# Optimization experiments

Measured on AMD Instinct MI355X. Metric: run time of the kernel, lower is better.

The kernel has to match this reference:

```python
import jax, jax.numpy as jnp
import numpy as np

STDS = np.array([0.1, 0.1, 0.2, 0.2], np.float32)
MEANS = np.array([0.0, 0.0, 0.0, 0.0], np.float32)
NMS_THRESH = 0.3  # cfg.TEST.NMS


def _decode_clip(boxes, deltas, iminfo):
    # boxes [R,4] (x1,y1,x2,y2), deltas [R,C,4] (unnormalized), iminfo [3]=(h,w,scale)
    w = boxes[:, 2] - boxes[:, 0] + 1.0
    h = boxes[:, 3] - boxes[:, 1] + 1.0
    cx = boxes[:, 0] + 0.5 * w
    cy = boxes[:, 1] + 0.5 * h
    pcx = deltas[..., 0] * w[:, None] + cx[:, None]
    pcy = deltas[..., 1] * h[:, None] + cy[:, None]
    pw = jnp.exp(deltas[..., 2]) * w[:, None]
    ph = jnp.exp(deltas[..., 3]) * h[:, None]
    x1 = pcx - 0.5 * pw
    y1 = pcy - 0.5 * ph
    x2 = pcx + 0.5 * pw
    y2 = pcy + 0.5 * ph
    x1 = jnp.clip(x1, 0.0, iminfo[1] - 1.0)
    x2 = jnp.clip(x2, 0.0, iminfo[1] - 1.0)
    y1 = jnp.clip(y1, 0.0, iminfo[0] - 1.0)
    y2 = jnp.clip(y2, 0.0, iminfo[0] - 1.0)
    return jnp.stack([x1, y1, x2, y2], axis=-1)  # [R,C,4]


def _nms_keep(boxes, valid):
    # boxes [R,4] sorted by score desc; valid [R] bool. Greedy hard NMS, fixed shape.
    b = jax.lax.stop_gradient(boxes)
    R = b.shape[0]
    x1, y1, x2, y2 = b[:, 0], b[:, 1], b[:, 2], b[:, 3]
    area = jnp.maximum(x2 - x1, 0.0) * jnp.maximum(y2 - y1, 0.0)
    xx1 = jnp.maximum(x1[:, None], x1[None, :])
    yy1 = jnp.maximum(y1[:, None], y1[None, :])
    xx2 = jnp.minimum(x2[:, None], x2[None, :])
    yy2 = jnp.minimum(y2[:, None], y2[None, :])
    inter = jnp.maximum(xx2 - xx1, 0.0) * jnp.maximum(yy2 - yy1, 0.0)
    iou = inter / (area[:, None] + area[None, :] - inter + 1e-9)
    ar = jnp.arange(R)
    def body(i, keep):
        sup = (iou[i] > NMS_THRESH) & (ar > i) & keep[i]
        return keep & ~sup
    return jax.lax.fori_loop(0, R, body, valid)


def _per_class(scores, boxes, thresh, cls_id):
    # scores [R], boxes [R,4], scalar thresh, scalar class id
    valid = scores > thresh
    s = jnp.where(valid, scores, -jnp.inf)
    order = jnp.argsort(-s)
    b = boxes[order]
    v = valid[order]
    keep = _nms_keep(b, v)
    dets = jnp.concatenate([b, jnp.full((b.shape[0], 1), cls_id, b.dtype)], axis=1)  # [R,5]
    return dets, keep


def _per_image(scores, pred_boxes, thr, num_pad):
    # scores [R,C], pred_boxes [R,C,4], thr [C]
    C = scores.shape[1]
    cls_ids = jnp.arange(1, C, dtype=scores.dtype)
    dets, keep = jax.vmap(_per_class, in_axes=(1, 1, 0, 0))(
        scores[:, 1:], pred_boxes[:, 1:], thr[1:], cls_ids)  # [C-1,R,5], [C-1,R]
    dets = dets.reshape(-1, 5)   # class-major order == torch.cat over classes
    keep = keep.reshape(-1)
    pos = jnp.cumsum(keep) - 1
    write = keep & (pos < num_pad)  # truncate to num_pad like the original
    idx = jnp.where(write, pos, num_pad)  # overflow bucket
    out = jnp.zeros((num_pad + 1, 5), dets.dtype).at[idx].add(
        dets * write[:, None].astype(dets.dtype))
    n = jnp.minimum(keep.sum(), num_pad)
    return out[:num_pad], n  # zero-padded [num_pad,5], count


def reference(cls_prob, rois, bbox_pred, im_info, per_class_threshold, num_classes):
    B, R, C = cls_prob.shape
    deltas = bbox_pred.reshape(B, R, C, 4) * STDS + MEANS
    pred = jax.vmap(_decode_clip)(rois[:, :, 1:5], deltas, im_info)  # [B,R,C,4]
    gt, n = jax.vmap(lambda s, p: _per_image(s, p, per_class_threshold, num_classes))(
        cls_prob, pred)
    return gt, n


def setup_inputs() -> dict:
    key = jax.random.key(0)
    B, R, C = 2, 1000, 81
    ks = jax.random.split(key, 6)
    cls_prob = jax.nn.softmax(2.0 * jax.random.normal(ks[0], (B, R, C)), axis=-1)
    cx = jax.random.uniform(ks[1], (B, R)) * 1200.0 + 50.0
    cy = jax.random.uniform(ks[2], (B, R)) * 700.0 + 50.0
    bw = jax.random.uniform(ks[3], (B, R)) * 300.0 + 16.0
    bh = jax.random.uniform(ks[4], (B, R)) * 300.0 + 16.0
    x1 = jnp.clip(cx - 0.5 * bw, 0.0, 1332.0)
    x2 = jnp.clip(cx + 0.5 * bw, 0.0, 1332.0)
    y1 = jnp.clip(cy - 0.5 * bh, 0.0, 799.0)
    y2 = jnp.clip(cy + 0.5 * bh, 0.0, 799.0)
    rois = jnp.concatenate([jnp.zeros((B, R, 1)), jnp.stack([x1, y1, x2, y2], -1)], -1)
    bbox_pred = 0.5 * jax.random.normal(ks[5], (B, R, 4 * C))
    im_info = jnp.tile(jnp.array([[800.0, 1333.0, 1.0]], jnp.float32), (B, 1))
    per_class_threshold = jnp.full((C,), 0.05, jnp.float32)
    return {"cls_prob": cls_prob, "rois": rois, "bbox_pred": bbox_pred,
            "im_info": im_info, "per_class_threshold": per_class_threshold,
            "num_classes": C}
```

## Files before the change

### kernel.cpp

```cpp
#include <hip/hip_runtime.h>
#include <math.h>

#define MAXC 256
#define NMS_T 0.3f

__global__ __launch_bounds__(256) void nms_fused_kernel(
    const float* __restrict__ cls_prob, const float* __restrict__ rois,
    const float* __restrict__ bbox_pred, const float* __restrict__ im_info,
    const float* __restrict__ thr, float* __restrict__ ws_boxes,
    int* __restrict__ ws_counts, float* __restrict__ gt,
    float* __restrict__ nout, int B, int R, int C)
{
    const int task = blockIdx.x;
    const int NC = C - 1;
    const int b = task / NC;
    const int c = 1 + (task % NC);
    const int tid = threadIdx.x;
    const int lane = tid & 63;
    const unsigned long long lane_lt = (1ull << lane) - 1ull;

    __shared__ float2 s_pair[MAXC];
    __shared__ float4 s_bx[MAXC];
    __shared__ float  s_area[MAXC];
    __shared__ unsigned long long s_keepw[4];
    __shared__ int s_cnt;
    __shared__ int s_flag;
    __shared__ int s_pcnt[128];
    __shared__ int s_poff[128];
    __shared__ int s_total;

    if (tid == 0) s_cnt = 0;
    __syncthreads();

    const float tc = thr[c];
    for (int r = tid; r < R; r += 256) {
        float s = cls_prob[((size_t)b * R + r) * C + c];
        if (s > tc) {
            int p = atomicAdd(&s_cnt, 1);
            if (p < MAXC) s_pair[p] = make_float2(s, __int_as_float(r));
        }
    }
    __syncthreads();
    int K = s_cnt; if (K > MAXC) K = MAXC;

    const float maxx = im_info[b * 3 + 1] - 1.0f;
    const float maxy = im_info[b * 3 + 0] - 1.0f;

    if (tid < K) {
        const float2 me = s_pair[tid];
        const float si = me.x;
        const int   ri = __float_as_int(me.y);
        int rank = 0;
        for (int j = 0; j < K; j++) {
            float2 pj = s_pair[j];
            rank += (pj.x > si) || (pj.x == si && __float_as_int(pj.y) < ri);
        }
        const float* rp = rois + ((size_t)b * R + ri) * 5;
        float rx1 = rp[1], ry1 = rp[2], rx2 = rp[3], ry2 = rp[4];
        float w  = rx2 - rx1 + 1.0f;
        float h  = ry2 - ry1 + 1.0f;
        float cx = rx1 + 0.5f * w;
        float cy = ry1 + 0.5f * h;
        const float4 dv = *(const float4*)(bbox_pred + (((size_t)b * R + ri) * C + c) * 4);
        float d0 = dv.x * 0.1f, d1 = dv.y * 0.1f;
        float d2 = dv.z * 0.2f, d3 = dv.w * 0.2f;
        float pcx = d0 * w + cx;
        float pcy = d1 * h + cy;
        float pw  = expf(d2) * w;
        float ph  = expf(d3) * h;
        float x1 = fminf(fmaxf(pcx - 0.5f * pw, 0.0f), maxx);
        float x2 = fminf(fmaxf(pcx + 0.5f * pw, 0.0f), maxx);
        float y1 = fminf(fmaxf(pcy - 0.5f * ph, 0.0f), maxy);
        float y2 = fminf(fmaxf(pcy + 0.5f * ph, 0.0f), maxy);
        s_bx[rank] = make_float4(x1, y1, x2, y2);
        s_area[rank] = fmaxf(x2 - x1, 0.0f) * fmaxf(y2 - y1, 0.0f);
    }
    __syncthreads();

    float* dst = ws_boxes + (size_t)task * C * 5;
    const float cid = (float)c;

    if (K <= 64) {
        if (tid < 64) {
            float4 bj = (lane < K) ? s_bx[lane] : make_float4(0.f, 0.f, 0.f, 0.f);
            float  aj = (lane < K) ? s_area[lane] : 0.0f;
            unsigned long long row = 0ull;
            for (int j = 0; j < K; j++) {
                float4 bb = s_bx[j];
                float  ab = s_area[j];
                float xx1 = fmaxf(bj.x, bb.x);
                float yy1 = fmaxf(bj.y, bb.y);
                float xx2 = fminf(bj.z, bb.z);
                float yy2 = fminf(bj.w, bb.w);
                float inter = fmaxf(xx2 - xx1, 0.0f) * fmaxf(yy2 - yy1, 0.0f);
                float iou = inter / (aj + ab - inter + 1e-9f);
                if (j > lane && iou > NMS_T) row |= (1ull << j);
            }
            unsigned int rlo32 = (unsigned int)(row & 0xffffffffull);
            unsigned int rhi32 = (unsigned int)(row >> 32);
            unsigned long long rem = (K >= 64) ? ~0ull
                                   : ((K > 0) ? ((1ull << K) - 1ull) : 0ull);
            unsigned long long keep = 0ull;
            while (rem) {
                int i = __builtin_ctzll(rem);
                keep |= (1ull << i);
                unsigned int lo = (unsigned int)__shfl((int)rlo32, i);
                unsigned int hi = (unsigned int)__shfl((int)rhi32, i);
                rem &= ~(((unsigned long long)hi << 32) | lo);
                rem &= ~(1ull << i);
            }
            if ((keep >> lane) & 1ull) {
                int pos = __popcll(keep & lane_lt);
                if (pos < C) {
                    dst[pos * 5 + 0] = bj.x;
                    dst[pos * 5 + 1] = bj.y;
                    dst[pos * 5 + 2] = bj.z;
                    dst[pos * 5 + 3] = bj.w;
                    dst[pos * 5 + 4] = cid;
                }
            }
            if (lane == 0) ws_counts[task] = __popcll(keep);
        }
    } else {
        int q = tid >> 6;
        int idx = q * 64 + lane;
        float4 bq = (idx < K) ? s_bx[idx] : make_float4(0.f, 0.f, 0.f, 0.f);
        float  aq = (idx < K) ? s_area[idx] : 0.0f;
        if (tid < 4) {
            int remk = K - tid * 64;
            s_keepw[tid] = (remk >= 64) ? ~0ull
                         : ((remk > 0) ? ((1ull << remk) - 1ull) : 0ull);
        }
        __syncthreads();
        for (int i = 0; i < K; i++) {
            if ((s_keepw[i >> 6] >> (i & 63)) & 1ull) {
                float4 bi = s_bx[i];
                float  ai = s_area[i];
                float xx1 = fmaxf(bi.x, bq.x);
                float yy1 = fmaxf(bi.y, bq.y);
                float xx2 = fminf(bi.z, bq.z);
                float yy2 = fminf(bi.w, bq.w);
                float inter = fmaxf(xx2 - xx1, 0.0f) * fmaxf(yy2 - yy1, 0.0f);
                float iou = inter / (ai + aq - inter + 1e-9f);
                bool sup = (idx < K) && (idx > i) && (iou > NMS_T);
                unsigned long long supm = __ballot(sup);
                if (supm && lane == 0) s_keepw[q] &= ~supm;
            }
            __syncthreads();
        }
        unsigned long long km = s_keepw[q];
        int base = 0;
        for (int w = 0; w < q; w++) base += __popcll(s_keepw[w]);
        if (idx < K && ((km >> lane) & 1ull)) {
            int pos = base + __popcll(km & lane_lt);
            if (pos < C) {
                dst[pos * 5 + 0] = bq.x;
                dst[pos * 5 + 1] = bq.y;
                dst[pos * 5 + 2] = bq.z;
                dst[pos * 5 + 3] = bq.w;
                dst[pos * 5 + 4] = cid;
            }
        }
        if (tid == 0) {
            int total = 0;
#pragma unroll
            for (int w = 0; w < 4; w++) total += __popcll(s_keepw[w]);
            ws_counts[task] = total;
        }
    }

    __syncthreads();
    __threadfence();
    if (tid == 0) {
        unsigned int old = atomicAdd((unsigned int*)&nout[b], 1u);
        s_flag = (old == (unsigned int)(NC - 1)) ||
                 (old == 0xAAAAAAAAu + (unsigned int)(NC - 1));
    }
    __syncthreads();
    if (!s_flag) return;
    __threadfence();

    const int P = C;
    if (tid < NC) s_pcnt[tid] = ws_counts[b * NC + tid];
    __syncthreads();
    if (tid < NC) {
        int acc = 0;
        for (int cc = 0; cc < NC; cc++) {
            int v = s_pcnt[cc];
            if (cc < tid) acc += v;
        }
        s_poff[tid] = acc;
        if (tid == NC - 1) s_total = acc + s_pcnt[tid];
    }
    __syncthreads();
    const int n = (s_total < P) ? s_total : P;

    for (int i = n * 5 + tid; i < P * 5; i += 256)
        gt[(size_t)b * P * 5 + i] = 0.0f;

    if (tid < n) {
        int pos = tid;
        int lo = 0, hi = NC - 1;
        while (lo < hi) {
            int mid = (lo + hi + 1) >> 1;
            if (s_poff[mid] <= pos) lo = mid; else hi = mid - 1;
        }
        int cc = lo;
        int k = pos - s_poff[cc];
        const float* src = ws_boxes + (((size_t)(b * NC + cc)) * P + k) * 5;
        float4 v = *(const float4*)src;
        float  v4 = src[4];
        float* d = gt + ((size_t)b * P + pos) * 5;
        d[0] = v.x; d[1] = v.y; d[2] = v.z; d[3] = v.w; d[4] = v4;
    }
    if (tid == 0) nout[b] = (float)n;
}

extern "C" void kernel_launch(void* const* d_in, const int* in_sizes, int n_in,
                              void* d_out, int out_size, void* d_ws, size_t ws_size,
                              hipStream_t stream) {
    const float* cls_prob  = (const float*)d_in[0];
    const float* rois      = (const float*)d_in[1];
    const float* bbox_pred = (const float*)d_in[2];
    const float* im_info   = (const float*)d_in[3];
    const float* thr       = (const float*)d_in[4];

    const int B = in_sizes[3] / 3;
    const int C = in_sizes[4];
    const int R = in_sizes[0] / (B * C);
    const int NC = C - 1;

    float* ws_boxes = (float*)d_ws;
    int*   ws_counts = (int*)(ws_boxes + (size_t)B * NC * C * 5);

    float* gt   = (float*)d_out;
    float* nout = (float*)d_out + (size_t)B * C * 5;

    nms_fused_kernel<<<B * NC, 256, 0, stream>>>(
        cls_prob, rois, bbox_pred, im_info, thr, ws_boxes, ws_counts,
        gt, nout, B, R, C);
}
```

Before: 95.58 us.

## Add single-wave bitmask NMS path for up to 128 candidates and batch score loads

Adds a K<=128 path where one wavefront computes suppression bitmasks for two boxes per lane and resolves greedy NMS through shuffle loops. This replaces the block-wide per-candidate loop that needed a __syncthreads per iteration. Score loads are unrolled four per thread so more memory requests are in flight at once. The gt zero-fill moves from the last-finishing block to the first block of each image. It also relies on ordering between blocks: the zero-fill must complete before the finishing block writes, with no explicit synchronization.

```diff
diff --git a/kernel.cpp b/kernel.cpp
--- a/kernel.cpp
+++ b/kernel.cpp
@@ -18,6 +18,7 @@
     const int tid = threadIdx.x;
     const int lane = tid & 63;
     const unsigned long long lane_lt = (1ull << lane) - 1ull;
+    const int P = C;
 
     __shared__ float2 s_pair[MAXC];
     __shared__ float4 s_bx[MAXC];
@@ -30,14 +31,28 @@
     __shared__ int s_total;
 
     if (tid == 0) s_cnt = 0;
+
+    if (task == b * NC) {
+        for (int i = tid; i < P * 5; i += 256)
+            gt[(size_t)b * P * 5 + i] = 0.0f;
+    }
     __syncthreads();
 
     const float tc = thr[c];
-    for (int r = tid; r < R; r += 256) {
-        float s = cls_prob[((size_t)b * R + r) * C + c];
-        if (s > tc) {
-            int p = atomicAdd(&s_cnt, 1);
-            if (p < MAXC) s_pair[p] = make_float2(s, __int_as_float(r));
+    for (int r0 = 0; r0 < R; r0 += 1024) {
+        float v[4];
+#pragma unroll
+        for (int k = 0; k < 4; k++) {
+            int r = r0 + k * 256 + tid;
+            v[k] = (r < R) ? cls_prob[((size_t)b * R + r) * C + c] : -1.0f;
+        }
+#pragma unroll
+        for (int k = 0; k < 4; k++) {
+            int r = r0 + k * 256 + tid;
+            if (v[k] > tc) {
+                int p = atomicAdd(&s_cnt, 1);
+                if (p < MAXC) s_pair[p] = make_float2(v[k], __int_as_float(r));
+            }
         }
     }
     __syncthreads();
@@ -96,18 +111,14 @@
                 float iou = inter / (aj + ab - inter + 1e-9f);
                 if (j > lane && iou > NMS_T) row |= (1ull << j);
             }
-            unsigned int rlo32 = (unsigned int)(row & 0xffffffffull);
-            unsigned int rhi32 = (unsigned int)(row >> 32);
             unsigned long long rem = (K >= 64) ? ~0ull
                                    : ((K > 0) ? ((1ull << K) - 1ull) : 0ull);
             unsigned long long keep = 0ull;
             while (rem) {
                 int i = __builtin_ctzll(rem);
                 keep |= (1ull << i);
-                unsigned int lo = (unsigned int)__shfl((int)rlo32, i);
-                unsigned int hi = (unsigned int)__shfl((int)rhi32, i);
-                rem &= ~(((unsigned long long)hi << 32) | lo);
                 rem &= ~(1ull << i);
+                rem &= ~__shfl(row, i);
             }
             if ((keep >> lane) & 1ull) {
                 int pos = __popcll(keep & lane_lt);
@@ -120,6 +131,70 @@
                 }
             }
             if (lane == 0) ws_counts[task] = __popcll(keep);
+        }
+    } else if (K <= 128) {
+        if (tid < 64) {
+            float4 b0 = s_bx[lane];
+            float  a0 = s_area[lane];
+            const int i1 = 64 + lane;
+            float4 b1 = (i1 < K) ? s_bx[i1] : make_float4(0.f, 0.f, 0.f, 0.f);
+            float  a1 = (i1 < K) ? s_area[i1] : 0.0f;
+            unsigned long long r0lo = 0, r0hi = 0, r1hi = 0;
+            for (int j = 0; j < K; j++) {
+                float4 bb = s_bx[j];
+                float  ab = s_area[j];
+                float xx1 = fmaxf(b0.x, bb.x), yy1 = fmaxf(b0.y, bb.y);
+                float xx2 = fminf(b0.z, bb.z), yy2 = fminf(b0.w, bb.w);
+                float in0 = fmaxf(xx2 - xx1, 0.0f) * fmaxf(yy2 - yy1, 0.0f);
+                float iou0 = in0 / (a0 + ab - in0 + 1e-9f);
+                float ux1 = fmaxf(b1.x, bb.x), uy1 = fmaxf(b1.y, bb.y);
+                float ux2 = fminf(b1.z, bb.z), uy2 = fminf(b1.w, bb.w);
+                float in1 = fmaxf(ux2 - ux1, 0.0f) * fmaxf(uy2 - uy1, 0.0f);
+                float iou1 = in1 / (a1 + ab - in1 + 1e-9f);
+                unsigned long long bit = 1ull << (j & 63);
+                bool sup0 = (j > lane) && (iou0 > NMS_T);
+                bool sup1 = (j > i1) && (iou1 > NMS_T);
+                if (j < 64) { if (sup0) r0lo |= bit; }
+                else        { if (sup0) r0hi |= bit; if (sup1) r1hi |= bit; }
+            }
+            unsigned long long rem0 = ~0ull;
+            unsigned long long rem1 = (K >= 128) ? ~0ull : ((1ull << (K - 64)) - 1ull);
+            unsigned long long keep0 = 0, keep1 = 0;
+            while (rem0) {
+                int i = __builtin_ctzll(rem0);
+                keep0 |= (1ull << i);
+                rem0 &= ~(1ull << i);
+                rem0 &= ~__shfl(r0lo, i);
+                rem1 &= ~__shfl(r0hi, i);
+            }
+            while (rem1) {
+                int i = __builtin_ctzll(rem1);
+                keep1 |= (1ull << i);
+                rem1 &= ~(1ull << i);
+                rem1 &= ~__shfl(r1hi, i);
+            }
+            int n0 = __popcll(keep0);
+            if ((keep0 >> lane) & 1ull) {
+                int pos = __popcll(keep0 & lane_lt);
+                if (pos < C) {
+                    dst[pos * 5 + 0] = b0.x;
+                    dst[pos * 5 + 1] = b0.y;
+                    dst[pos * 5 + 2] = b0.z;
+                    dst[pos * 5 + 3] = b0.w;
+                    dst[pos * 5 + 4] = cid;
+                }
+            }
+            if (i1 < K && ((keep1 >> lane) & 1ull)) {
+                int pos = n0 + __popcll(keep1 & lane_lt);
+                if (pos < C) {
+                    dst[pos * 5 + 0] = b1.x;
+                    dst[pos * 5 + 1] = b1.y;
+                    dst[pos * 5 + 2] = b1.z;
+                    dst[pos * 5 + 3] = b1.w;
+                    dst[pos * 5 + 4] = cid;
+                }
+            }
+            if (lane == 0) ws_counts[task] = n0 + __popcll(keep1);
         }
     } else {
         int q = tid >> 6;
@@ -180,7 +255,6 @@
     if (!s_flag) return;
     __threadfence();
 
-    const int P = C;
     if (tid < NC) s_pcnt[tid] = ws_counts[b * NC + tid];
     __syncthreads();
     if (tid < NC) {
@@ -194,9 +268,6 @@
     }
     __syncthreads();
     const int n = (s_total < P) ? s_total : P;
-
-    for (int i = n * 5 + tid; i < P * 5; i += 256)
-        gt[(size_t)b * P * 5 + i] = 0.0f;
 
     if (tid < n) {
         int pos = tid;
```

After: 94.45 us. About the same (-1.2%).
